# Optimization experiments

Measured on AMD Instinct MI355X. Metric: run time of the kernel, lower is better.

The kernel has to match this reference:

```python
import jax, jax.numpy as jnp
import numpy as np

B = 4        # samples
GP = 6       # graphs per sample (K*2)
N = 1024     # nodes per graph
DIN = 128    # input feature dim
D = 128      # out_channels
E = 16384    # edges per graph


def setup_inputs() -> dict:
    k = jax.random.split(jax.random.key(0), 10)
    G = B * GP
    s = 0.05
    return {
        "x": jax.random.normal(k[0], (G, N, DIN), jnp.float32),
        "edge_attr": jax.random.uniform(k[1], (G, E, 6), jnp.float32),
        "gcn_W": jax.random.normal(k[2], (4, DIN, D), jnp.float32) * s,
        "gcn_b": jnp.zeros((4, D), jnp.float32),
        "Ws": jax.random.normal(k[3], (4, D, D), jnp.float32) * s,
        "lin1_W": jax.random.normal(k[4], (GP * D, 20), jnp.float32) * s,
        "lin1_b": jnp.zeros((20,), jnp.float32),
        "codefc_W": jax.random.normal(k[5], (20, 2), jnp.float32) * s,
        "codefc_b": jnp.zeros((2,), jnp.float32),
        "lin2_W": jax.random.normal(k[6], (GP * D, GP), jnp.float32) * s,
        "lin2_b": jnp.zeros((GP,), jnp.float32),
        "simfc_W": jax.random.normal(k[7], (GP, 2), jnp.float32) * s,
        "simfc_b": jnp.zeros((2,), jnp.float32),
        "edge_index": jax.random.randint(k[8], (G, 2, E), 0, N, jnp.int64),
    }


def _gcn(x, src, dst, ew, W, b):
    # PyG GCNConv with normalize=True, add_self_loops=True (self-loop weight 1)
    n = x.shape[0]
    deg = jax.ops.segment_sum(ew, dst, num_segments=n) + 1.0
    dinv = jax.lax.rsqrt(deg)
    xw = x @ W
    norm = dinv[src] * ew * dinv[dst]               # [E]
    agg = jax.ops.segment_sum(norm[:, None] * xw[src], dst, num_segments=n)
    return agg + (dinv * dinv)[:, None] * xw + b    # self-loop term + bias


def _gnnlayer(x, ei, ea, gcn_W, gcn_b, Ws):
    # x_tmp = sum_i relu(GCN_i(x, ew=edge_attr[:, i+2])) @ Ws[i]
    src, dst = ei[0], ei[1]
    def chan(W, b, Wmix, ew):
        return jnp.maximum(_gcn(x, src, dst, ew, W, b), 0.0) @ Wmix
    return jax.vmap(chan)(gcn_W, gcn_b, Ws, ea[:, 2:6].T).sum(0)  # [N, D]


def _forward(x, edge_attr, gcn_W, gcn_b, Ws, lin1_W, lin1_b, codefc_W,
             codefc_b, lin2_W, lin2_b, simfc_W, simfc_b, edge_index):
    # per-graph GNN layer over all G = B*GP graphs
    x_tmp = jax.vmap(lambda xg, eig, eag: _gnnlayer(xg, eig, eag, gcn_W, gcn_b, Ws))(
        x, edge_index, edge_attr)                    # [G, N, D]
    g = x_tmp.mean(axis=1).reshape(B, GP * D)        # g_matrix [B, 768]
    # L2-normalize rows (F.normalize eps=1e-12)
    xn = x_tmp / jnp.clip(jnp.linalg.norm(x_tmp, axis=-1, keepdims=True), 1e-12)
    xn = xn.reshape(B, GP, N, D)
    # all-pairs cosine sim -> tanh -> 21-bin histogram on [-1, 1] -> weighted sum
    S = jnp.tanh(jnp.einsum('bind,bjmd->bijnm', xn, xn))   # [B,GP,GP,N,N]
    idx = jnp.clip(jnp.floor((S + 1.0) * (21.0 / 2.0)).astype(jnp.int32), 0, 20)
    centers = jnp.linspace(-1.0, 1.0, 21, dtype=jnp.float32)
    # hist/(N*N) dot centers == mean of per-element bin centers
    sim = centers[idx].mean(axis=(3, 4))             # [B, GP, GP]
    # backnet
    feat = jnp.maximum(g @ lin1_W + lin1_b, 0.0)     # feature_of_G [B, 20]
    code = jax.nn.log_softmax(feat @ codefc_W + codefc_b, axis=1)
    strength = g @ lin2_W + lin2_b                   # [B, GP]
    sim_res = jax.nn.log_softmax((sim.mean(axis=2) * strength) @ simfc_W + simfc_b, axis=1)
    r = 0.4 * code + 0.6 * sim_res
    return r, feat


def reference(x, edge_attr, gcn_W, gcn_b, Ws, lin1_W, lin1_b, codefc_W,
              codefc_b, lin2_W, lin2_b, simfc_W, simfc_b, edge_index):
    return _forward(x, edge_attr, gcn_W, gcn_b, Ws, lin1_W, lin1_b, codefc_W,
                    codefc_b, lin2_W, lin2_b, simfc_W, simfc_b, edge_index)
```

## Files before the change

### kernel.cpp

```cpp
#include <hip/hip_runtime.h>

#define NG 24
#define NB 4
#define GPg 6
#define NN 1024
#define DD 128
#define EE 16384

typedef __bf16 bf16;
typedef __bf16 bf16x8 __attribute__((ext_vector_type(8)));
typedef float f32x4 __attribute__((ext_vector_type(4)));

#define GLOBAL_AS __attribute__((address_space(1)))
#define LDS_AS __attribute__((address_space(3)))

__device__ __forceinline__ int binidx(float v) {
  float u = v * v;
  float q = fmaf(fmaf(fmaf(-0.261093f, u, 1.222977f), u, -3.463278f), u, 10.49874f);
  return (int)fmaf(v, q, 10.5f);
}

__global__ void k_zero(f32x4* __restrict__ p) {
  int i = blockIdx.x * 256 + threadIdx.x;
  if (i < 6948) p[i] = f32x4{0.f, 0.f, 0.f, 0.f};
}

__global__ void k_histw(const int* __restrict__ ei, int* __restrict__ counts,
                        const float* __restrict__ gW, const float* __restrict__ Ws,
                        bf16* __restrict__ gwt, bf16* __restrict__ wst) {
  int bid = blockIdx.x;
  if (bid >= 1536) {
    int i = (bid - 1536) * 256 + threadIdx.x;
    int c = i >> 14, k = (i >> 7) & 127, j = i & 127;
    gwt[(c << 14) | (j << 7) | k] = (bf16)gW[i];
    wst[(j << 9) | (c << 7) | k] = (bf16)Ws[i];
    return;
  }
  int t = bid * 256 + threadIdx.x;
  int g = t >> 14, e = t & (EE - 1);
  int dst = ei[g * 2 * EE + EE + e];
  atomicAdd(&counts[g * NN + dst], 1);
}

__global__ void k_scan(const int* __restrict__ counts, int* __restrict__ offs,
                       int* __restrict__ cursor) {
  __shared__ int wsum[16];
  int g = blockIdx.x, t = threadIdx.x;
  int lane = t & 63, wv = t >> 6;
  int myc = counts[g * NN + t];
  int v = myc;
#pragma unroll
  for (int d = 1; d < 64; d <<= 1) {
    int u = __shfl_up(v, d);
    if (lane >= d) v += u;
  }
  if (lane == 63) wsum[wv] = v;
  __syncthreads();
  if (t < 16) {
    int s = wsum[t];
#pragma unroll
    for (int d = 1; d < 16; d <<= 1) {
      int u = __shfl_up(s, d);
      if (t >= d) s += u;
    }
    wsum[t] = s;
  }
  __syncthreads();
  int incl = v + (wv > 0 ? wsum[wv - 1] : 0);
  int excl = incl - myc;
  offs[g * 1025 + t] = excl;
  cursor[g * NN + t] = excl;
  if (t == NN - 1) offs[g * 1025 + NN] = incl;
}

__global__ void k_scatter(const int* __restrict__ ei, int* __restrict__ cursor,
                          int* __restrict__ csrs) {
  int t = blockIdx.x * 256 + threadIdx.x;
  if (t >= NG * EE) return;
  int g = t >> 14, e = t & (EE - 1);
  int src = ei[g * 2 * EE + e], dst = ei[g * 2 * EE + EE + e];
  int pos = atomicAdd(&cursor[g * NN + dst], 1);
  csrs[(size_t)g * EE + pos] = src | (e << 10);
}

__global__ void k_deg(const int* __restrict__ offs, const int* __restrict__ csrs,
                      const float* __restrict__ ea, float* __restrict__ dinv4) {
  int t = blockIdx.x * 256 + threadIdx.x;
  int c = t & 3, n = (t >> 2) & (NN - 1), g = t >> 12;
  int beg = offs[g * 1025 + n], end = offs[g * 1025 + n + 1];
  const int* sp = csrs + (size_t)g * EE;
  const float* eag = ea + (size_t)g * EE * 6 + 2 + c;
  float s = 1.0f;
  for (int p = beg; p < end; ++p) {
    int e = sp[p] >> 10;
    s += eag[(size_t)e * 6];
  }
  dinv4[t] = rsqrtf(s);
}

__global__ __launch_bounds__(256) void k_xw(const float* __restrict__ x,
                                            const bf16* __restrict__ gwt,
                                            const float* __restrict__ dinv4,
                                            bf16* __restrict__ xw) {
  int bid = blockIdx.x;
  int gc = bid >> 3, mb = bid & 7;
  int g = gc >> 2, c = gc & 3;
  int lane = threadIdx.x & 63, wid = threadIdx.x >> 6;
  int wm = wid >> 1, wn = wid & 1;
  int row0 = mb * 128 + wm * 64, col0 = wn * 64;
  const float* A = x + (size_t)g * NN * DD;
  const bf16* Bt = gwt + (size_t)c * DD * DD;
  int lr = lane & 15, lk = (lane >> 4) * 8;
  f32x4 acc[4][4] = {};
  for (int kc = 0; kc < 128; kc += 32) {
    bf16x8 a[4], b[4];
#pragma unroll
    for (int i2 = 0; i2 < 4; i2++) {
      const f32x4* pa = (const f32x4*)(A + (size_t)(row0 + i2 * 16 + lr) * DD + kc + lk);
      f32x4 f0 = pa[0], f1 = pa[1];
#pragma unroll
      for (int q = 0; q < 4; q++) { a[i2][q] = (bf16)f0[q]; a[i2][4 + q] = (bf16)f1[q]; }
    }
#pragma unroll
    for (int j2 = 0; j2 < 4; j2++)
      b[j2] = *(const bf16x8*)(Bt + (size_t)(col0 + j2 * 16 + lr) * DD + kc + lk);
#pragma unroll
    for (int i2 = 0; i2 < 4; i2++)
#pragma unroll
      for (int j2 = 0; j2 < 4; j2++)
        acc[i2][j2] = __builtin_amdgcn_mfma_f32_16x16x32_bf16(a[i2], b[j2], acc[i2][j2], 0, 0, 0);
  }
  bf16* out = xw + (size_t)g * NN * 512 + c * 128;
  const float* dv = dinv4 + ((size_t)g * NN) * 4 + c;
  int cr = (lane >> 4) * 4, cc = lane & 15;
#pragma unroll
  for (int i2 = 0; i2 < 4; i2++)
#pragma unroll
    for (int r2 = 0; r2 < 4; r2++) {
      int row = row0 + i2 * 16 + cr + r2;
      float dvv = dv[row * 4];
#pragma unroll
      for (int j2 = 0; j2 < 4; j2++)
        out[(size_t)row * 512 + col0 + j2 * 16 + cc] = (bf16)(acc[i2][j2][r2] * dvv);
    }
}

__global__ __launch_bounds__(256) void k_agg(const int* __restrict__ offs, const int* __restrict__ csrs,
                                             const float* __restrict__ ea, const float* __restrict__ dinv4,
                                             const float* __restrict__ gb, const bf16* __restrict__ xw,
                                             bf16* __restrict__ hb) {
  int bid = blockIdx.x;
  int lb = (bid & 7) * (NG * 256 / 8) + (bid >> 3);
  int g = lb >> 8, n4 = lb & 255;
  int wid = threadIdx.x >> 6, lane = threadIdx.x & 63;
  int n = n4 * 4 + wid;
  int c = lane >> 4, d0 = (lane & 15) * 8;
  const bf16* xwg = xw + (size_t)g * NN * 512;
  int beg = offs[g * 1025 + n], end = offs[g * 1025 + n + 1];
  const int* sp = csrs + (size_t)g * EE;
  const float* eag = ea + (size_t)g * EE * 6 + 2 + c;
  float dvn = dinv4[((size_t)g * NN + n) * 4 + c];
  float acc[8] = {};
  int p = beg;
  for (; p + 3 < end; p += 4) {
    int u0 = sp[p], u1 = sp[p + 1], u2 = sp[p + 2], u3 = sp[p + 3];
    int s0 = u0 & 1023, s1 = u1 & 1023, s2 = u2 & 1023, s3 = u3 & 1023;
    float w0 = eag[(size_t)(u0 >> 10) * 6];
    float w1 = eag[(size_t)(u1 >> 10) * 6];
    float w2 = eag[(size_t)(u2 >> 10) * 6];
    float w3 = eag[(size_t)(u3 >> 10) * 6];
    bf16x8 v0 = *(const bf16x8*)(xwg + (size_t)s0 * 512 + lane * 8);
    bf16x8 v1 = *(const bf16x8*)(xwg + (size_t)s1 * 512 + lane * 8);
    bf16x8 v2 = *(const bf16x8*)(xwg + (size_t)s2 * 512 + lane * 8);
    bf16x8 v3 = *(const bf16x8*)(xwg + (size_t)s3 * 512 + lane * 8);
#pragma unroll
    for (int q = 0; q < 8; q++)
      acc[q] += w0 * (float)v0[q] + w1 * (float)v1[q] + w2 * (float)v2[q] + w3 * (float)v3[q];
  }
  for (; p < end; ++p) {
    int u0 = sp[p];
    int s0 = u0 & 1023;
    float w0 = eag[(size_t)(u0 >> 10) * 6];
    bf16x8 v0 = *(const bf16x8*)(xwg + (size_t)s0 * 512 + lane * 8);
#pragma unroll
    for (int q = 0; q < 8; q++) acc[q] += w0 * (float)v0[q];
  }
  bf16x8 vs = *(const bf16x8*)(xwg + (size_t)n * 512 + lane * 8);
  bf16x8 o;
#pragma unroll
  for (int q = 0; q < 8; q++) {
    float r2 = dvn * (acc[q] + (float)vs[q]) + gb[c * 128 + d0 + q];
    o[q] = (bf16)fmaxf(r2, 0.f);
  }
  *(bf16x8*)(hb + ((size_t)g * NN + n) * 512 + lane * 8) = o;
}

__global__ __launch_bounds__(256) void k_mixn(const bf16* __restrict__ hb,
                                              const bf16* __restrict__ wst,
                                              float* __restrict__ gmat,
                                              bf16* __restrict__ xn) {
  __shared__ float rowssq[64];
  int bid = blockIdx.x;
  int g = bid >> 4, mb = bid & 15;
  int lane = threadIdx.x & 63, wid = threadIdx.x >> 6;
  int wm = wid >> 1, wn = wid & 1;
  int row0 = mb * 64 + wm * 32, col0 = wn * 64;
  const bf16* H = hb + (size_t)g * NN * 512;
  int lr = lane & 15, lk = (lane >> 4) * 8;
  if (threadIdx.x < 64) rowssq[threadIdx.x] = 0.f;
  f32x4 acc[2][4] = {};
  for (int kc = 0; kc < 512; kc += 32) {
    bf16x8 a[2], b[4];
#pragma unroll
    for (int i2 = 0; i2 < 2; i2++)
      a[i2] = *(const bf16x8*)(H + (size_t)(row0 + i2 * 16 + lr) * 512 + kc + lk);
#pragma unroll
    for (int j2 = 0; j2 < 4; j2++)
      b[j2] = *(const bf16x8*)(wst + (size_t)(col0 + j2 * 16 + lr) * 512 + kc + lk);
#pragma unroll
    for (int i2 = 0; i2 < 2; i2++)
#pragma unroll
      for (int j2 = 0; j2 < 4; j2++)
        acc[i2][j2] = __builtin_amdgcn_mfma_f32_16x16x32_bf16(a[i2], b[j2], acc[i2][j2], 0, 0, 0);
  }
  __syncthreads();
  int cr = (lane >> 4) * 4, cc = lane & 15;
#pragma unroll
  for (int i2 = 0; i2 < 2; i2++)
#pragma unroll
    for (int r2 = 0; r2 < 4; r2++) {
      float s = 0.f;
#pragma unroll
      for (int j2 = 0; j2 < 4; j2++) { float v = acc[i2][j2][r2]; s += v * v; }
#pragma unroll
      for (int d2 = 1; d2 < 16; d2 <<= 1) s += __shfl_xor(s, d2);
      if (cc == 0) atomicAdd(&rowssq[wm * 32 + i2 * 16 + cr + r2], s);
    }
#pragma unroll
  for (int j2 = 0; j2 < 4; j2++) {
    float s = 0.f;
#pragma unroll
    for (int i2 = 0; i2 < 2; i2++)
#pragma unroll
      for (int r2 = 0; r2 < 4; r2++) s += acc[i2][j2][r2];
    s += __shfl_xor(s, 16);
    s += __shfl_xor(s, 32);
    if ((lane >> 4) == 0)
      atomicAdd(&gmat[(g / GPg) * 768 + (g % GPg) * 128 + col0 + j2 * 16 + cc], s * (1.0f / NN));
  }
  __syncthreads();
  bf16* xp = xn + (size_t)g * NN * DD;
#pragma unroll
  for (int i2 = 0; i2 < 2; i2++)
#pragma unroll
    for (int r2 = 0; r2 < 4; r2++) {
      int rowl = wm * 32 + i2 * 16 + cr + r2;
      float inv = 1.0f / fmaxf(sqrtf(rowssq[rowl]), 1e-12f);
#pragma unroll
      for (int j2 = 0; j2 < 4; j2++)
        xp[(size_t)(mb * 64 + rowl) * DD + col0 + j2 * 16 + cc] = (bf16)(acc[i2][j2][r2] * inv);
    }
}

__global__ __launch_bounds__(256, 4) void k_pair(const bf16* __restrict__ xn,
                                                 unsigned* __restrict__ simsum) {
  __shared__ char lds[16384];
  int bid = blockIdx.x;
  int lb = (bid & 7) * 168 + (bid >> 3);
  int b = lb / 336, rem = lb % 336;
  int pj = rem >> 4, rem2 = rem & 15;
  int s128 = rem2 >> 1, half = rem2 & 1;
  int r = pj, i = 0;
  while (r >= 6 - i) { r -= 6 - i; ++i; }
  int j = i + r;
  bool isdiag = (i == j);
  int tb = half * 16, te = tb + 16;
  if (isdiag && 4 * s128 > tb) tb = 4 * s128;
  if (tb >= te) return;
  int lane = threadIdx.x & 63, wid = threadIdx.x >> 6;
  int lr = lane & 15, hi16 = (lane >> 4) * 16;
  const char* Ag = (const char*)(xn + ((size_t)(b * GPg + i) * NN + s128 * 128 + wid * 32) * DD);
  const char* Bg0 = (const char*)(xn + (size_t)(b * GPg + j) * NN * DD);

  bf16x8 a[2][4];
#pragma unroll
  for (int g2 = 0; g2 < 2; g2++)
#pragma unroll
    for (int kc = 0; kc < 4; kc++) {
      a[g2][kc] = *(const bf16x8*)(Ag + (g2 * 16 + lr) * 256 + kc * 64 + hi16);
      asm volatile("" :: "v"(a[g2][kc]));
    }

  auto stage = [&](int buf, int tn) {
    const char* src = Bg0 + tn * 8192;
#pragma unroll
    for (int j2 = 0; j2 < 2; ++j2)
      __builtin_amdgcn_global_load_lds(
          (const GLOBAL_AS void*)(src + (j2 * 16 + lr) * 256 + wid * 64 + hi16),
          (LDS_AS void*)(lds + buf * 8192 + wid * 2048 + j2 * 1024), 16, 0, 0);
  };
  stage(0, tb);
  if (tb + 1 < te) stage(1, tb + 1);

  int cnt = 0;
  int cc = lane & 15, cr = (lane >> 4) * 4;
  for (int t = tb; t < te; ++t) {
    int cur = (t - tb) & 1;
    if (t < te - 1) asm volatile("s_waitcnt vmcnt(2)" ::: "memory");
    else            asm volatile("s_waitcnt vmcnt(0)" ::: "memory");
    __builtin_amdgcn_s_barrier();
    const char* Bl = lds + cur * 8192;
    f32x4 acc[2][2] = {};
#pragma unroll
    for (int kc = 0; kc < 4; kc++) {
      bf16x8 bb[2];
#pragma unroll
      for (int j2 = 0; j2 < 2; j2++)
        bb[j2] = *(const bf16x8*)(Bl + kc * 2048 + j2 * 1024 + lane * 16);
#pragma unroll
      for (int g2 = 0; g2 < 2; g2++)
#pragma unroll
        for (int j2 = 0; j2 < 2; j2++)
          acc[g2][j2] = __builtin_amdgcn_mfma_f32_16x16x32_bf16(a[g2][kc], bb[j2], acc[g2][j2], 0, 0, 0);
    }
    asm volatile("s_waitcnt lgkmcnt(0)" ::: "memory");
    __builtin_amdgcn_sched_barrier(0);
    __builtin_amdgcn_s_barrier();
    if (t + 2 < te) stage(cur, t + 2);
    if (isdiag && t < 4 * s128 + 4) {
      int tc = 0;
#pragma unroll
      for (int g2 = 0; g2 < 2; g2++)
#pragma unroll
        for (int j2 = 0; j2 < 2; j2++)
#pragma unroll
          for (int r2 = 0; r2 < 4; r2++) {
            int idx = binidx(acc[g2][j2][r2]);
            int lm = t * 32 + j2 * 16 + cc;
            int ln = s128 * 128 + wid * 32 + g2 * 16 + cr + r2;
            tc += (lm > ln) ? 2 * idx : (lm == ln ? idx : 0);
          }
      cnt += tc;
    } else {
      int tc = 0;
#pragma unroll
      for (int g2 = 0; g2 < 2; g2++)
#pragma unroll
        for (int j2 = 0; j2 < 2; j2++)
#pragma unroll
          for (int r2 = 0; r2 < 4; r2++)
            tc += binidx(acc[g2][j2][r2]);
      cnt += isdiag ? 2 * tc : tc;
    }
  }
#pragma unroll
  for (int d2 = 32; d2; d2 >>= 1) cnt += __shfl_xor(cnt, d2);
  if (lane == 0) atomicAdd(&simsum[((size_t)b * GPg + i) * GPg + j], (unsigned)cnt);
}

__global__ void k_back(const float* __restrict__ gmat, const unsigned* __restrict__ simsum,
                       const float* __restrict__ l1W, const float* __restrict__ l1b,
                       const float* __restrict__ cfW, const float* __restrict__ cfb,
                       const float* __restrict__ l2W, const float* __restrict__ l2b,
                       const float* __restrict__ sfW, const float* __restrict__ sfb,
                       float* __restrict__ out) {
  __shared__ float feat[NB][20];
  __shared__ float strength[NB][GPg];
  __shared__ float simmean[NB][GPg];
  int t = threadIdx.x, g = t >> 3, l = t & 7;
  if (g < 80) {
    int b = g / 20, jj = g % 20;
    float s = 0.f;
#pragma unroll 8
    for (int k = l; k < 768; k += 8) s += gmat[b * 768 + k] * l1W[k * 20 + jj];
    s += __shfl_xor(s, 1); s += __shfl_xor(s, 2); s += __shfl_xor(s, 4);
    if (l == 0) {
      float f = fmaxf(s + l1b[jj], 0.f);
      feat[b][jj] = f;
      out[8 + b * 20 + jj] = f;
    }
  } else if (g < 104) {
    int q = g - 80, b = q / GPg, pp = q % GPg;
    float s = 0.f;
#pragma unroll 8
    for (int k = l; k < 768; k += 8) s += gmat[b * 768 + k] * l2W[k * GPg + pp];
    s += __shfl_xor(s, 1); s += __shfl_xor(s, 2); s += __shfl_xor(s, 4);
    if (l == 0) strength[b][pp] = s + l2b[pp];
  } else if (t >= 832 && t < 856) {
    int q = t - 832; int b = q / GPg, ii = q % GPg;
    float s = 0.f;
    for (int jj = 0; jj < GPg; jj++) {
      int lo = ii < jj ? ii : jj, hi = ii < jj ? jj : ii;
      s += -1.0f + 0.1f * (float)simsum[(b * GPg + lo) * GPg + hi] * (1.0f / (1024.f * 1024.f));
    }
    simmean[b][ii] = s * (1.0f / GPg);
  }
  __syncthreads();
  if (t < NB) {
    int b = t;
    float l1v[2], l2v[2];
#pragma unroll
    for (int u = 0; u < 2; u++) {
      float s = cfb[u];
      for (int jj = 0; jj < 20; jj++) s += feat[b][jj] * cfW[jj * 2 + u];
      l1v[u] = s;
      float s2 = sfb[u];
      for (int pp = 0; pp < GPg; pp++) s2 += simmean[b][pp] * strength[b][pp] * sfW[pp * 2 + u];
      l2v[u] = s2;
    }
    float m1 = fmaxf(l1v[0], l1v[1]);
    float lse1 = m1 + logf(expf(l1v[0] - m1) + expf(l1v[1] - m1));
    float m2 = fmaxf(l2v[0], l2v[1]);
    float lse2 = m2 + logf(expf(l2v[0] - m2) + expf(l2v[1] - m2));
    out[b * 2 + 0] = 0.4f * (l1v[0] - lse1) + 0.6f * (l2v[0] - lse2);
    out[b * 2 + 1] = 0.4f * (l1v[1] - lse1) + 0.6f * (l2v[1] - lse2);
  }
}

extern "C" void kernel_launch(void* const* d_in, const int* in_sizes, int n_in,
                              void* d_out, int out_size, void* d_ws, size_t ws_size,
                              hipStream_t stream) {
  const float* x   = (const float*)d_in[0];
  const float* ea  = (const float*)d_in[1];
  const float* gW  = (const float*)d_in[2];
  const float* gb  = (const float*)d_in[3];
  const float* Ws  = (const float*)d_in[4];
  const float* l1W = (const float*)d_in[5];
  const float* l1b = (const float*)d_in[6];
  const float* cfW = (const float*)d_in[7];
  const float* cfb = (const float*)d_in[8];
  const float* l2W = (const float*)d_in[9];
  const float* l2b = (const float*)d_in[10];
  const float* sfW = (const float*)d_in[11];
  const float* sfb = (const float*)d_in[12];
  const int* eidx  = (const int*)d_in[13];
  float* out = (float*)d_out;

  char* w = (char*)d_ws;
  auto alloc = [&](size_t bytes) { char* p = w; w += (bytes + 255) & ~(size_t)255; return (void*)p; };
  bf16* gwt     = (bf16*)alloc(4 * DD * DD * 2);
  bf16* wst     = (bf16*)alloc(4 * DD * DD * 2);
  int* counts   = (int*)alloc((size_t)NG * NN * 4);
  float* gmat   = (float*)alloc((size_t)NB * 768 * 4);
  unsigned* simsum = (unsigned*)alloc((size_t)NB * 36 * 4);
  float* dinv4  = (float*)alloc((size_t)NG * NN * 4 * 4);
  int* offs     = (int*)alloc((size_t)NG * 1025 * 4);
  int* cursor   = (int*)alloc((size_t)NG * NN * 4);
  int* csrs     = (int*)alloc((size_t)NG * EE * 4);
  bf16* xw      = (bf16*)alloc((size_t)NG * NN * 512 * 2);
  bf16* hb      = (bf16*)alloc((size_t)NG * NN * 512 * 2);
  bf16* xn      = (bf16*)alloc((size_t)NG * NN * DD * 2);

  k_zero<<<28, 256, 0, stream>>>((f32x4*)counts);
  k_histw<<<1792, 256, 0, stream>>>(eidx, counts, gW, Ws, gwt, wst);
  k_scan<<<NG, 1024, 0, stream>>>(counts, offs, cursor);
  k_scatter<<<(NG * EE) / 256, 256, 0, stream>>>(eidx, cursor, csrs);
  k_deg<<<(NG * NN * 4) / 256, 256, 0, stream>>>(offs, csrs, ea, dinv4);
  k_xw<<<NG * 4 * 8, 256, 0, stream>>>(x, gwt, dinv4, xw);
  k_agg<<<NG * 256, 256, 0, stream>>>(offs, csrs, ea, dinv4, gb, xw, hb);
  k_mixn<<<NG * 16, 256, 0, stream>>>(hb, wst, gmat, xn);
  k_pair<<<1344, 256, 0, stream>>>(xn, simsum);
  k_back<<<1, 1024, 0, stream>>>(gmat, simsum, l1W, l1b, cfW, cfb, l2W, l2b, sfW, sfb, out);
}
```

Measured before the change: 185.3 us.

## Double k_pair block to 512 threads covering 256 rows per staged tile

The pairwise similarity kernel now uses 8 waves per block, each owning 32 query rows, so every block covers 256 rows of graph i against each staged 32-row B tile. Each wave issues a single global-to-LDS load per tile, which halves the B staging traffic per row of output. Diagonal blocks now skip per-wave tiles below the diagonal and apply the triangular mask only on the wave's own diagonal tile, which trims wasted MFMA work. In exchange the block is larger with no occupancy hint, and idle waves still have to join the barriers.

```diff
diff --git a/kernel.cpp b/kernel.cpp
--- a/kernel.cpp
+++ b/kernel.cpp
@@ -262,24 +262,25 @@
     }
 }
 
-__global__ __launch_bounds__(256, 4) void k_pair(const bf16* __restrict__ xn,
-                                                 unsigned* __restrict__ simsum) {
+__global__ __launch_bounds__(512) void k_pair(const bf16* __restrict__ xn,
+                                              unsigned* __restrict__ simsum) {
   __shared__ char lds[16384];
   int bid = blockIdx.x;
-  int lb = (bid & 7) * 168 + (bid >> 3);
-  int b = lb / 336, rem = lb % 336;
-  int pj = rem >> 4, rem2 = rem & 15;
-  int s128 = rem2 >> 1, half = rem2 & 1;
+  int lb = (bid & 7) * 84 + (bid >> 3);
+  int b = lb / 168, rem = lb % 168;
+  int pj = rem >> 3, rem2 = rem & 7;
+  int s256 = rem2 >> 1, half = rem2 & 1;
   int r = pj, i = 0;
   while (r >= 6 - i) { r -= 6 - i; ++i; }
   int j = i + r;
   bool isdiag = (i == j);
   int tb = half * 16, te = tb + 16;
-  if (isdiag && 4 * s128 > tb) tb = 4 * s128;
+  if (isdiag && 8 * s256 > tb) tb = 8 * s256;
   if (tb >= te) return;
   int lane = threadIdx.x & 63, wid = threadIdx.x >> 6;
   int lr = lane & 15, hi16 = (lane >> 4) * 16;
-  const char* Ag = (const char*)(xn + ((size_t)(b * GPg + i) * NN + s128 * 128 + wid * 32) * DD);
+  int dtile = s256 * 8 + wid;
+  const char* Ag = (const char*)(xn + ((size_t)(b * GPg + i) * NN + s256 * 256 + wid * 32) * DD);
   const char* Bg0 = (const char*)(xn + (size_t)(b * GPg + j) * NN * DD);
 
   bf16x8 a[2][4];
@@ -291,13 +292,12 @@
       asm volatile("" :: "v"(a[g2][kc]));
     }
 
+  int kc_s = wid >> 1, j2_s = wid & 1;
+  int gsrc = (j2_s * 16 + lr) * 256 + kc_s * 64 + hi16;
   auto stage = [&](int buf, int tn) {
-    const char* src = Bg0 + tn * 8192;
-#pragma unroll
-    for (int j2 = 0; j2 < 2; ++j2)
-      __builtin_amdgcn_global_load_lds(
-          (const GLOBAL_AS void*)(src + (j2 * 16 + lr) * 256 + wid * 64 + hi16),
-          (LDS_AS void*)(lds + buf * 8192 + wid * 2048 + j2 * 1024), 16, 0, 0);
+    __builtin_amdgcn_global_load_lds(
+        (const GLOBAL_AS void*)(Bg0 + tn * 8192 + gsrc),
+        (LDS_AS void*)(lds + buf * 8192 + wid * 1024), 16, 0, 0);
   };
   stage(0, tb);
   if (tb + 1 < te) stage(1, tb + 1);
@@ -306,28 +306,32 @@
   int cc = lane & 15, cr = (lane >> 4) * 4;
   for (int t = tb; t < te; ++t) {
     int cur = (t - tb) & 1;
-    if (t < te - 1) asm volatile("s_waitcnt vmcnt(2)" ::: "memory");
+    if (t < te - 1) asm volatile("s_waitcnt vmcnt(1)" ::: "memory");
     else            asm volatile("s_waitcnt vmcnt(0)" ::: "memory");
     __builtin_amdgcn_s_barrier();
-    const char* Bl = lds + cur * 8192;
+    bool act = !isdiag || (t >= dtile);
     f32x4 acc[2][2] = {};
-#pragma unroll
-    for (int kc = 0; kc < 4; kc++) {
-      bf16x8 bb[2];
-#pragma unroll
-      for (int j2 = 0; j2 < 2; j2++)
-        bb[j2] = *(const bf16x8*)(Bl + kc * 2048 + j2 * 1024 + lane * 16);
-#pragma unroll
-      for (int g2 = 0; g2 < 2; g2++)
+    if (act) {
+      const char* Bl = lds + cur * 8192;
+#pragma unroll
+      for (int kc = 0; kc < 4; kc++) {
+        bf16x8 bb[2];
 #pragma unroll
         for (int j2 = 0; j2 < 2; j2++)
-          acc[g2][j2] = __builtin_amdgcn_mfma_f32_16x16x32_bf16(a[g2][kc], bb[j2], acc[g2][j2], 0, 0, 0);
-    }
-    asm volatile("s_waitcnt lgkmcnt(0)" ::: "memory");
-    __builtin_amdgcn_sched_barrier(0);
+          bb[j2] = *(const bf16x8*)(Bl + kc * 2048 + j2 * 1024 + lane * 16);
+#pragma unroll
+        for (int g2 = 0; g2 < 2; g2++)
+#pragma unroll
+          for (int j2 = 0; j2 < 2; j2++)
+            acc[g2][j2] = __builtin_amdgcn_mfma_f32_16x16x32_bf16(a[g2][kc], bb[j2], acc[g2][j2], 0, 0, 0);
+      }
+      asm volatile("s_waitcnt lgkmcnt(0)" ::: "memory");
+      __builtin_amdgcn_sched_barrier(0);
+    }
     __builtin_amdgcn_s_barrier();
     if (t + 2 < te) stage(cur, t + 2);
-    if (isdiag && t < 4 * s128 + 4) {
+    if (!act) continue;
+    if (isdiag && t == dtile) {
       int tc = 0;
 #pragma unroll
       for (int g2 = 0; g2 < 2; g2++)
@@ -336,8 +340,8 @@
 #pragma unroll
           for (int r2 = 0; r2 < 4; r2++) {
             int idx = binidx(acc[g2][j2][r2]);
-            int lm = t * 32 + j2 * 16 + cc;
-            int ln = s128 * 128 + wid * 32 + g2 * 16 + cr + r2;
+            int lm = j2 * 16 + cc;
+            int ln = g2 * 16 + cr + r2;
             tc += (lm > ln) ? 2 * idx : (lm == ln ? idx : 0);
           }
       cnt += tc;
@@ -355,7 +359,7 @@
   }
 #pragma unroll
   for (int d2 = 32; d2; d2 >>= 1) cnt += __shfl_xor(cnt, d2);
-  if (lane == 0) atomicAdd(&simsum[((size_t)b * GPg + i) * GPg + j], (unsigned)cnt);
+  if (lane == 0 && cnt != 0) atomicAdd(&simsum[((size_t)b * GPg + i) * GPg + j], (unsigned)cnt);
 }
 
 __global__ void k_back(const float* __restrict__ gmat, const unsigned* __restrict__ simsum,
@@ -459,6 +463,6 @@
   k_xw<<<NG * 4 * 8, 256, 0, stream>>>(x, gwt, dinv4, xw);
   k_agg<<<NG * 256, 256, 0, stream>>>(offs, csrs, ea, dinv4, gb, xw, hb);
   k_mixn<<<NG * 16, 256, 0, stream>>>(hb, wst, gmat, xn);
-  k_pair<<<1344, 256, 0, stream>>>(xn, simsum);
+  k_pair<<<672, 512, 0, stream>>>(xn, simsum);
   k_back<<<1, 1024, 0, stream>>>(gmat, simsum, l1W, l1b, cfW, cfb, l2W, l2b, sfW, sfb, out);
 }
```

Result: slower. 195.4 us (+5.5%).

## Decouple XW GEMM from degree norm and fuse it with edge histogram

Applied to the files above, without the earlier changes.

The XW GEMM no longer scales rows by the source-node dinv, so it can run in the same launch as the edge-count histogram, before scan, scatter and degree computation. The source dinv scaling moves into the aggregation kernel as an extra gathered load per edge. The self-loop term now gets dinv squared. The counter zeroing and the weight transposes are merged into one small launch. This removes a launch and lets the GEMM overlap with the atomic histogram, at the cost of extra scattered dinv reads in the aggregation.

```diff
diff --git a/kernel.cpp b/kernel.cpp
--- a/kernel.cpp
+++ b/kernel.cpp
@@ -20,26 +20,71 @@
   return (int)fmaf(v, q, 10.5f);
 }
 
-__global__ void k_zero(f32x4* __restrict__ p) {
-  int i = blockIdx.x * 256 + threadIdx.x;
-  if (i < 6948) p[i] = f32x4{0.f, 0.f, 0.f, 0.f};
-}
-
-__global__ void k_histw(const int* __restrict__ ei, int* __restrict__ counts,
-                        const float* __restrict__ gW, const float* __restrict__ Ws,
-                        bf16* __restrict__ gwt, bf16* __restrict__ wst) {
+__global__ void k_zerow(f32x4* __restrict__ p, const float* __restrict__ gW,
+                        const float* __restrict__ Ws, bf16* __restrict__ gwt,
+                        bf16* __restrict__ wst) {
   int bid = blockIdx.x;
-  if (bid >= 1536) {
-    int i = (bid - 1536) * 256 + threadIdx.x;
-    int c = i >> 14, k = (i >> 7) & 127, j = i & 127;
-    gwt[(c << 14) | (j << 7) | k] = (bf16)gW[i];
-    wst[(j << 9) | (c << 7) | k] = (bf16)Ws[i];
+  if (bid < 28) {
+    int i = bid * 256 + threadIdx.x;
+    if (i < 6948) p[i] = f32x4{0.f, 0.f, 0.f, 0.f};
     return;
   }
-  int t = bid * 256 + threadIdx.x;
-  int g = t >> 14, e = t & (EE - 1);
-  int dst = ei[g * 2 * EE + EE + e];
-  atomicAdd(&counts[g * NN + dst], 1);
+  int i = (bid - 28) * 256 + threadIdx.x;
+  int c = i >> 14, k = (i >> 7) & 127, j = i & 127;
+  gwt[(c << 14) | (j << 7) | k] = (bf16)gW[i];
+  wst[(j << 9) | (c << 7) | k] = (bf16)Ws[i];
+}
+
+__global__ __launch_bounds__(256) void k_histxw(const int* __restrict__ ei, int* __restrict__ counts,
+                                                const float* __restrict__ x, const bf16* __restrict__ gwt,
+                                                bf16* __restrict__ xw) {
+  int bid = blockIdx.x;
+  if (bid < 1536) {
+    int t = bid * 256 + threadIdx.x;
+    int g = t >> 14, e = t & (EE - 1);
+    int dst = ei[g * 2 * EE + EE + e];
+    atomicAdd(&counts[g * NN + dst], 1);
+    return;
+  }
+  int xb = bid - 1536;
+  int gc = xb >> 3, mb = xb & 7;
+  int g = gc >> 2, c = gc & 3;
+  int lane = threadIdx.x & 63, wid = threadIdx.x >> 6;
+  int wm = wid >> 1, wn = wid & 1;
+  int row0 = mb * 128 + wm * 64, col0 = wn * 64;
+  const float* A = x + (size_t)g * NN * DD;
+  const bf16* Bt = gwt + (size_t)c * DD * DD;
+  int lr = lane & 15, lk = (lane >> 4) * 8;
+  f32x4 acc[4][4] = {};
+  for (int kc = 0; kc < 128; kc += 32) {
+    bf16x8 a[4], b[4];
+#pragma unroll
+    for (int i2 = 0; i2 < 4; i2++) {
+      const f32x4* pa = (const f32x4*)(A + (size_t)(row0 + i2 * 16 + lr) * DD + kc + lk);
+      f32x4 f0 = pa[0], f1 = pa[1];
+#pragma unroll
+      for (int q = 0; q < 4; q++) { a[i2][q] = (bf16)f0[q]; a[i2][4 + q] = (bf16)f1[q]; }
+    }
+#pragma unroll
+    for (int j2 = 0; j2 < 4; j2++)
+      b[j2] = *(const bf16x8*)(Bt + (size_t)(col0 + j2 * 16 + lr) * DD + kc + lk);
+#pragma unroll
+    for (int i2 = 0; i2 < 4; i2++)
+#pragma unroll
+      for (int j2 = 0; j2 < 4; j2++)
+        acc[i2][j2] = __builtin_amdgcn_mfma_f32_16x16x32_bf16(a[i2], b[j2], acc[i2][j2], 0, 0, 0);
+  }
+  bf16* out = xw + (size_t)g * NN * 512 + c * 128;
+  int cr = (lane >> 4) * 4, cc = lane & 15;
+#pragma unroll
+  for (int i2 = 0; i2 < 4; i2++)
+#pragma unroll
+    for (int r2 = 0; r2 < 4; r2++) {
+      int row = row0 + i2 * 16 + cr + r2;
+#pragma unroll
+      for (int j2 = 0; j2 < 4; j2++)
+        out[(size_t)row * 512 + col0 + j2 * 16 + cc] = (bf16)acc[i2][j2][r2];
+    }
 }
 
 __global__ void k_scan(const int* __restrict__ counts, int* __restrict__ offs,
@@ -96,53 +141,6 @@
     s += eag[(size_t)e * 6];
   }
   dinv4[t] = rsqrtf(s);
-}
-
-__global__ __launch_bounds__(256) void k_xw(const float* __restrict__ x,
-                                            const bf16* __restrict__ gwt,
-                                            const float* __restrict__ dinv4,
-                                            bf16* __restrict__ xw) {
-  int bid = blockIdx.x;
-  int gc = bid >> 3, mb = bid & 7;
-  int g = gc >> 2, c = gc & 3;
-  int lane = threadIdx.x & 63, wid = threadIdx.x >> 6;
-  int wm = wid >> 1, wn = wid & 1;
-  int row0 = mb * 128 + wm * 64, col0 = wn * 64;
-  const float* A = x + (size_t)g * NN * DD;
-  const bf16* Bt = gwt + (size_t)c * DD * DD;
-  int lr = lane & 15, lk = (lane >> 4) * 8;
-  f32x4 acc[4][4] = {};
-  for (int kc = 0; kc < 128; kc += 32) {
-    bf16x8 a[4], b[4];
-#pragma unroll
-    for (int i2 = 0; i2 < 4; i2++) {
-      const f32x4* pa = (const f32x4*)(A + (size_t)(row0 + i2 * 16 + lr) * DD + kc + lk);
-      f32x4 f0 = pa[0], f1 = pa[1];
-#pragma unroll
-      for (int q = 0; q < 4; q++) { a[i2][q] = (bf16)f0[q]; a[i2][4 + q] = (bf16)f1[q]; }
-    }
-#pragma unroll
-    for (int j2 = 0; j2 < 4; j2++)
-      b[j2] = *(const bf16x8*)(Bt + (size_t)(col0 + j2 * 16 + lr) * DD + kc + lk);
-#pragma unroll
-    for (int i2 = 0; i2 < 4; i2++)
-#pragma unroll
-      for (int j2 = 0; j2 < 4; j2++)
-        acc[i2][j2] = __builtin_amdgcn_mfma_f32_16x16x32_bf16(a[i2], b[j2], acc[i2][j2], 0, 0, 0);
-  }
-  bf16* out = xw + (size_t)g * NN * 512 + c * 128;
-  const float* dv = dinv4 + ((size_t)g * NN) * 4 + c;
-  int cr = (lane >> 4) * 4, cc = lane & 15;
-#pragma unroll
-  for (int i2 = 0; i2 < 4; i2++)
-#pragma unroll
-    for (int r2 = 0; r2 < 4; r2++) {
-      int row = row0 + i2 * 16 + cr + r2;
-      float dvv = dv[row * 4];
-#pragma unroll
-      for (int j2 = 0; j2 < 4; j2++)
-        out[(size_t)row * 512 + col0 + j2 * 16 + cc] = (bf16)(acc[i2][j2][r2] * dvv);
-    }
 }
 
 __global__ __launch_bounds__(256) void k_agg(const int* __restrict__ offs, const int* __restrict__ csrs,
@@ -159,16 +157,17 @@
   int beg = offs[g * 1025 + n], end = offs[g * 1025 + n + 1];
   const int* sp = csrs + (size_t)g * EE;
   const float* eag = ea + (size_t)g * EE * 6 + 2 + c;
-  float dvn = dinv4[((size_t)g * NN + n) * 4 + c];
+  const float* dvgc = dinv4 + ((size_t)g * NN) * 4 + c;
+  float dvn = dvgc[n * 4];
   float acc[8] = {};
   int p = beg;
   for (; p + 3 < end; p += 4) {
     int u0 = sp[p], u1 = sp[p + 1], u2 = sp[p + 2], u3 = sp[p + 3];
     int s0 = u0 & 1023, s1 = u1 & 1023, s2 = u2 & 1023, s3 = u3 & 1023;
-    float w0 = eag[(size_t)(u0 >> 10) * 6];
-    float w1 = eag[(size_t)(u1 >> 10) * 6];
-    float w2 = eag[(size_t)(u2 >> 10) * 6];
-    float w3 = eag[(size_t)(u3 >> 10) * 6];
+    float w0 = eag[(size_t)(u0 >> 10) * 6] * dvgc[s0 * 4];
+    float w1 = eag[(size_t)(u1 >> 10) * 6] * dvgc[s1 * 4];
+    float w2 = eag[(size_t)(u2 >> 10) * 6] * dvgc[s2 * 4];
+    float w3 = eag[(size_t)(u3 >> 10) * 6] * dvgc[s3 * 4];
     bf16x8 v0 = *(const bf16x8*)(xwg + (size_t)s0 * 512 + lane * 8);
     bf16x8 v1 = *(const bf16x8*)(xwg + (size_t)s1 * 512 + lane * 8);
     bf16x8 v2 = *(const bf16x8*)(xwg + (size_t)s2 * 512 + lane * 8);
@@ -180,7 +179,7 @@
   for (; p < end; ++p) {
     int u0 = sp[p];
     int s0 = u0 & 1023;
-    float w0 = eag[(size_t)(u0 >> 10) * 6];
+    float w0 = eag[(size_t)(u0 >> 10) * 6] * dvgc[s0 * 4];
     bf16x8 v0 = *(const bf16x8*)(xwg + (size_t)s0 * 512 + lane * 8);
 #pragma unroll
     for (int q = 0; q < 8; q++) acc[q] += w0 * (float)v0[q];
@@ -189,7 +188,7 @@
   bf16x8 o;
 #pragma unroll
   for (int q = 0; q < 8; q++) {
-    float r2 = dvn * (acc[q] + (float)vs[q]) + gb[c * 128 + d0 + q];
+    float r2 = dvn * (acc[q] + dvn * (float)vs[q]) + gb[c * 128 + d0 + q];
     o[q] = (bf16)fmaxf(r2, 0.f);
   }
   *(bf16x8*)(hb + ((size_t)g * NN + n) * 512 + lane * 8) = o;
@@ -451,12 +450,11 @@
   bf16* hb      = (bf16*)alloc((size_t)NG * NN * 512 * 2);
   bf16* xn      = (bf16*)alloc((size_t)NG * NN * DD * 2);
 
-  k_zero<<<28, 256, 0, stream>>>((f32x4*)counts);
-  k_histw<<<1792, 256, 0, stream>>>(eidx, counts, gW, Ws, gwt, wst);
+  k_zerow<<<284, 256, 0, stream>>>((f32x4*)counts, gW, Ws, gwt, wst);
+  k_histxw<<<2304, 256, 0, stream>>>(eidx, counts, x, gwt, xw);
   k_scan<<<NG, 1024, 0, stream>>>(counts, offs, cursor);
   k_scatter<<<(NG * EE) / 256, 256, 0, stream>>>(eidx, cursor, csrs);
   k_deg<<<(NG * NN * 4) / 256, 256, 0, stream>>>(offs, csrs, ea, dinv4);
-  k_xw<<<NG * 4 * 8, 256, 0, stream>>>(x, gwt, dinv4, xw);
   k_agg<<<NG * 256, 256, 0, stream>>>(offs, csrs, ea, dinv4, gb, xw, hb);
   k_mixn<<<NG * 16, 256, 0, stream>>>(hb, wst, gmat, xn);
   k_pair<<<1344, 256, 0, stream>>>(xn, simsum);
```

New measurement: 189.1 us. 1.02x slower.
